# Kernel optimization log

Hardware: AMD Instinct MI355X
Metric: run time of the kernel (lower is better)

The kernel has to match this reference:

```python
import jax, jax.numpy as jnp
import numpy as np

B, A, T, C = 16, 19200, 50, 80
LAMBDA_COORD = 5.0
EPS = 1e-6

def _make_boxes(key, shape):
    k1, k2 = jax.random.split(key)
    xy1 = jax.random.uniform(k1, shape[:-1] + (2,)) * 0.8
    wh = jax.random.uniform(k2, shape[:-1] + (2,)) * 0.2 + 0.01
    return jnp.concatenate([xy1, xy1 + wh], axis=-1)

def setup_inputs() -> dict:
    key = jax.random.key(0)
    ks = jax.random.split(key, 6)
    return {
        'pred_boxes': _make_boxes(ks[0], (B, A, 4)),
        'pred_conf': jax.random.normal(ks[1], (B, A, 1), dtype=jnp.float32),
        'pred_cls': jax.random.normal(ks[2], (B, A, C), dtype=jnp.float32),
        'target_boxes': _make_boxes(ks[3], (B, T, 4)),
        'target_labels': jax.random.randint(ks[4], (B, T), 0, C),
        'anchors': jax.random.uniform(ks[5], (3, 2), dtype=jnp.float32),
    }

def _bce_logits(x, z):
    # BCEWithLogits, reduction='none'
    return jnp.maximum(x, 0.0) - x * z + jnp.log1p(jnp.exp(-jnp.abs(x)))

def _box_iou(b1, b2):
    # b1: [A,4], b2: [T,4] -> [A,T]
    area1 = (b1[:, 2] - b1[:, 0]) * (b1[:, 3] - b1[:, 1])
    area2 = (b2[:, 2] - b2[:, 0]) * (b2[:, 3] - b2[:, 1])
    ix1 = jnp.maximum(b1[:, 0:1], b2[None, :, 0])
    iy1 = jnp.maximum(b1[:, 1:2], b2[None, :, 1])
    ix2 = jnp.minimum(b1[:, 2:3], b2[None, :, 2])
    iy2 = jnp.minimum(b1[:, 3:4], b2[None, :, 3])
    inter = jnp.clip(ix2 - ix1, 0.0) * jnp.clip(iy2 - iy1, 0.0)
    union = area1[:, None] + area2[None, :] - inter
    return inter / (union + EPS)

def _ciou_loss(b1, b2):
    # elementwise CIoU between matched boxes [T,4],[T,4]
    # (original builds pairwise IoU then takes the diagonal == elementwise IoU)
    area1 = (b1[:, 2] - b1[:, 0]) * (b1[:, 3] - b1[:, 1])
    area2 = (b2[:, 2] - b2[:, 0]) * (b2[:, 3] - b2[:, 1])
    iw = jnp.clip(jnp.minimum(b1[:, 2], b2[:, 2]) - jnp.maximum(b1[:, 0], b2[:, 0]), 0.0)
    ih = jnp.clip(jnp.minimum(b1[:, 3], b2[:, 3]) - jnp.maximum(b1[:, 1], b2[:, 1]), 0.0)
    inter = iw * ih
    iou = inter / (area1 + area2 - inter + EPS)
    b1x1, b1y1, b1x2, b1y2 = b1[:, 0], b1[:, 1], b1[:, 2], b1[:, 3]
    b2x1, b2y1, b2x2, b2y2 = b2[:, 0], b2[:, 1], b2[:, 2], b2[:, 3]
    c_diag = (jnp.maximum(b1x2, b2x2) - jnp.minimum(b1x1, b2x1)) ** 2 + \
             (jnp.maximum(b1y2, b2y2) - jnp.minimum(b1y1, b2y1)) ** 2
    center_dist = ((b1x1 + b1x2 - b2x1 - b2x2) / 2) ** 2 + ((b1y1 + b1y2 - b2y1 - b2y2) / 2) ** 2
    w1, h1 = b1x2 - b1x1, b1y2 - b1y1
    w2, h2 = b2x2 - b2x1, b2y2 - b2y1
    v = (4.0 / jnp.pi ** 2) * (jnp.arctan(w2 / h2) - jnp.arctan(w1 / h1)) ** 2
    alpha = v / (1.0 - iou + v + EPS)
    ciou = iou - center_dist / c_diag - alpha * v
    return 1.0 - ciou

def _per_image(pb, pc, pcls, tb, tl):
    # pb:[A,4] pc:[A,1] pcls:[A,C] tb:[T,4] tl:[T]
    ious = _box_iou(pb, tb)                    # [A,T]
    best_idx = jnp.argmax(ious, axis=0)        # [T]
    obj_mask = jnp.zeros((pb.shape[0], 1), pb.dtype).at[best_idx].set(1.0)
    obj_loss = _bce_logits(pc, obj_mask).mean()
    box_loss = _ciou_loss(pb[best_idx], tb).mean()
    tgt_cls = jax.nn.one_hot(tl, pcls.shape[-1], dtype=pcls.dtype)
    cls_loss = _bce_logits(pcls[best_idx], tgt_cls).mean()
    return box_loss, obj_loss, cls_loss

def reference(pred_boxes, pred_conf, pred_cls, target_boxes, target_labels, anchors):
    box_l, obj_l, cls_l = jax.vmap(_per_image)(pred_boxes, pred_conf, pred_cls, target_boxes, target_labels)
    bs = pred_boxes.shape[0]
    total_box = box_l.sum() / bs
    total_obj = obj_l.sum() / bs
    total_cls = cls_l.sum() / bs
    total = LAMBDA_COORD * total_box + total_obj + total_cls
    return total
```

## Files before the change

### kernel.cpp

```cpp
#include <hip/hip_runtime.h>
#include <math.h>

#define NB 16
#define NA 19200
#define NT 50
#define NC 80
#define LAMBDA_COORD 5.0f
#define F_EPS 1e-6f

#define TPG 5
#define NGRP (NT / TPG)
#define KA_BLOCKS (NB * NGRP)
#define KA_THREADS 1024
#define KA_WAVES (KA_THREADS / 64)
#define OBJ_F4_PER_BLK (NB * NA / 4 / KA_BLOCKS)

#define W_OBJ (1.0f / (float)(NB * NA))
#define W_BOX (LAMBDA_COORD / (float)(NB * NT))
#define W_CLS (1.0f / (float)(NB * NT * NC))


__device__ __forceinline__ float bce0(float x) {
    return fmaxf(x, 0.0f) + log1pf(expf(-fabsf(x)));
}

__global__ __launch_bounds__(1024) void kA(
        const float* __restrict__ pb,
        const float* __restrict__ pc,
        const float* __restrict__ pcls,
        const float* __restrict__ tb,
        const int* __restrict__ tl,
        int* __restrict__ best_idx,
        float* __restrict__ part) {
    const float4* pb4 = (const float4*)pb;
    const float4* tb4 = (const float4*)tb;
    const float4* pc4 = (const float4*)pc;

    const int b   = blockIdx.x / NGRP;
    const int g   = blockIdx.x % NGRP;
    const int tid = threadIdx.x;
    const int wave = tid >> 6;
    const int lane = tid & 63;

    float4 t4[TPG];
    float  ta[TPG];
    #pragma unroll
    for (int i = 0; i < TPG; ++i) {
        t4[i] = tb4[b * NT + g * TPG + i];
        ta[i] = (t4[i].z - t4[i].x) * (t4[i].w - t4[i].y) + F_EPS;
    }

    float best[TPG];
    int   bidx[TPG];
    #pragma unroll
    for (int i = 0; i < TPG; ++i) { best[i] = -1.0f; bidx[i] = NA; }

    const size_t boff = (size_t)b * NA;
    int a0 = tid;
    float4 p0 = pb4[boff + a0];
    int a1 = a0 + KA_THREADS;
    bool h1 = a1 < NA;
    float4 p1;
    if (h1) p1 = pb4[boff + a1];

    while (true) {
        const int a2 = a1 + KA_THREADS;
        const bool h2 = h1 && (a2 < NA);
        float4 p2;
        if (h2) p2 = pb4[boff + a2];

        {
            float area1 = (p0.z - p0.x) * (p0.w - p0.y);
            #pragma unroll
            for (int i = 0; i < TPG; ++i) {
                float ix1 = fmaxf(p0.x, t4[i].x), iy1 = fmaxf(p0.y, t4[i].y);
                float ix2 = fminf(p0.z, t4[i].z), iy2 = fminf(p0.w, t4[i].w);
                float inter = fmaxf(ix2 - ix1, 0.0f) * fmaxf(iy2 - iy1, 0.0f);
                float u = area1 + ta[i] - inter;
                float iou = inter * __builtin_amdgcn_rcpf(u);
                if (iou > best[i]) { best[i] = iou; bidx[i] = a0; }
            }
        }

        if (!h1) break;
        p0 = p1; a0 = a1;
        p1 = p2; a1 = a2; h1 = h2;
    }

    __shared__ float swv[KA_WAVES][TPG];
    __shared__ int   swi[KA_WAVES][TPG];
    __shared__ int   sbi5[TPG];
    __shared__ float swred[KA_WAVES];

    #pragma unroll
    for (int i = 0; i < TPG; ++i) {
        float v = best[i];
        int   ix = bidx[i];
        #pragma unroll
        for (int m = 1; m < 64; m <<= 1) {
            float ov = __shfl_xor(v, m);
            int   oi = __shfl_xor(ix, m);
            if (ov > v || (ov == v && oi < ix)) { v = ov; ix = oi; }
        }
        if (lane == 0) { swv[wave][i] = v; swi[wave][i] = ix; }
    }
    __syncthreads();

    if (tid < TPG) {
        float v = swv[0][tid];
        int   ix = swi[0][tid];
        #pragma unroll
        for (int w = 1; w < KA_WAVES; ++w) {
            float ov = swv[w][tid];
            int   oi = swi[w][tid];
            if (ov > v || (ov == v && oi < ix)) { v = ov; ix = oi; }
        }
        best_idx[b * NT + g * TPG + tid] = ix;
        sbi5[tid] = ix;
    }
    __syncthreads();

    float s = 0.0f;

    if (tid < TPG * NC) {
        const int t = tid / NC;
        const int c = tid - t * NC;
        float x = pcls[((size_t)b * NA + sbi5[t]) * NC + c];
        int lab = tl[b * NT + g * TPG + t];
        s += W_CLS * (bce0(x) - (lab == c ? x : 0.0f));
    }

    if (tid >= 512 && tid < 512 + TPG) {
        const int t  = tid - 512;
        const int bi = sbi5[t];
        const float* p  = pb + ((size_t)b * NA + bi) * 4;
        const float* tg = tb + ((size_t)b * NT + g * TPG + t) * 4;
        float b1x1 = p[0],  b1y1 = p[1],  b1x2 = p[2],  b1y2 = p[3];
        float b2x1 = tg[0], b2y1 = tg[1], b2x2 = tg[2], b2y2 = tg[3];

        float area1 = (b1x2 - b1x1) * (b1y2 - b1y1);
        float area2 = (b2x2 - b2x1) * (b2y2 - b2y1);
        float iw = fmaxf(fminf(b1x2, b2x2) - fmaxf(b1x1, b2x1), 0.0f);
        float ih = fmaxf(fminf(b1y2, b2y2) - fmaxf(b1y1, b2y1), 0.0f);
        float inter = iw * ih;
        float iou = inter / (area1 + area2 - inter + F_EPS);

        float cdx = fmaxf(b1x2, b2x2) - fminf(b1x1, b2x1);
        float cdy = fmaxf(b1y2, b2y2) - fminf(b1y1, b2y1);
        float c_diag = cdx * cdx + cdy * cdy;

        float cx = (b1x1 + b1x2 - b2x1 - b2x2) * 0.5f;
        float cy = (b1y1 + b1y2 - b2y1 - b2y2) * 0.5f;
        float center_dist = cx * cx + cy * cy;

        float w1 = b1x2 - b1x1, h1 = b1y2 - b1y1;
        float w2 = b2x2 - b2x1, h2 = b2y2 - b2y1;
        float dat = atanf(w2 / h2) - atanf(w1 / h1);
        float vv = (float)(4.0 / (M_PI * M_PI)) * dat * dat;
        float alpha = vv / (1.0f - iou + vv + F_EPS);
        float ciou = iou - center_dist / c_diag - alpha * vv;
        s += W_BOX * (1.0f - ciou);
    }

    if (tid < OBJ_F4_PER_BLK) {
        float4 v4 = pc4[blockIdx.x * OBJ_F4_PER_BLK + tid];
        s += W_OBJ * (bce0(v4.x) + bce0(v4.y) + bce0(v4.z) + bce0(v4.w));
    }

    #pragma unroll
    for (int m = 32; m > 0; m >>= 1) s += __shfl_down(s, m);
    if (lane == 0) swred[wave] = s;
    __syncthreads();
    if (tid < KA_WAVES) {
        float v = swred[tid];
        #pragma unroll
        for (int m = 8; m > 0; m >>= 1) v += __shfl_down(v, m);
        if (tid == 0) part[blockIdx.x] = v;
    }
}

__global__ __launch_bounds__(256) void kB(
        const float* __restrict__ pc,
        const int* __restrict__ best_idx,
        const float* __restrict__ part,
        float* __restrict__ out) {
    const int tid = threadIdx.x;
    const int wave = tid >> 6;
    const int lane = tid & 63;

    __shared__ int   sbi[NB * NT];
    __shared__ float swred[4];

    for (int i = tid; i < NB * NT; i += 256) sbi[i] = best_idx[i];
    __syncthreads();

    float s = 0.0f;
    if (tid < KA_BLOCKS) s += part[tid];

    for (int i = tid; i < NB * NT; i += 256) {
        const int b = i / NT;
        const int t = i - b * NT;
        const int bi = sbi[i];
        bool dup = false;
        for (int tp = 0; tp < t; ++tp)
            if (sbi[b * NT + tp] == bi) dup = true;
        if (!dup) s -= W_OBJ * pc[(size_t)b * NA + bi];
    }

    #pragma unroll
    for (int m = 32; m > 0; m >>= 1) s += __shfl_down(s, m);
    if (lane == 0) swred[wave] = s;
    __syncthreads();
    if (tid == 0) out[0] = swred[0] + swred[1] + swred[2] + swred[3];
}

extern "C" void kernel_launch(void* const* d_in, const int* in_sizes, int n_in,
                              void* d_out, int out_size, void* d_ws, size_t ws_size,
                              hipStream_t stream) {
    const float* pb   = (const float*)d_in[0];
    const float* pc   = (const float*)d_in[1];
    const float* pcls = (const float*)d_in[2];
    const float* tb   = (const float*)d_in[3];
    const int*   tl   = (const int*)d_in[4];

    char* ws = (char*)d_ws;
    float* part     = (float*)ws;
    int*   best_idx = (int*)(ws + 1024);

    kA<<<KA_BLOCKS, KA_THREADS, 0, stream>>>(pb, pc, pcls, tb, tl, best_idx, part);
    kB<<<1, 256, 0, stream>>>(pc, best_idx, part, (float*)d_out);
}
```

Before: 34.84 us.

## Split anchor scan into halves and move matched-loss work to per-batch second kernel

```diff
diff --git a/kernel.cpp b/kernel.cpp
--- a/kernel.cpp
+++ b/kernel.cpp
@@ -10,7 +10,9 @@
 
 #define TPG 5
 #define NGRP (NT / TPG)
-#define KA_BLOCKS (NB * NGRP)
+#define NHALF 2
+#define HALF_A (NA / NHALF)
+#define KA_BLOCKS (NB * NGRP * NHALF)
 #define KA_THREADS 1024
 #define KA_WAVES (KA_THREADS / 64)
 #define OBJ_F4_PER_BLK (NB * NA / 4 / KA_BLOCKS)
@@ -27,21 +29,26 @@
 __global__ __launch_bounds__(1024) void kA(
         const float* __restrict__ pb,
         const float* __restrict__ pc,
-        const float* __restrict__ pcls,
         const float* __restrict__ tb,
-        const int* __restrict__ tl,
-        int* __restrict__ best_idx,
-        float* __restrict__ part) {
+        float* __restrict__ val_part,
+        int* __restrict__ idx_part,
+        float* __restrict__ part,
+        float* __restrict__ out) {
     const float4* pb4 = (const float4*)pb;
     const float4* tb4 = (const float4*)tb;
     const float4* pc4 = (const float4*)pc;
 
-    const int b   = blockIdx.x / NGRP;
-    const int g   = blockIdx.x % NGRP;
+    const int blk = blockIdx.x;
+    const int b   = blk / (NGRP * NHALF);
+    const int r   = blk % (NGRP * NHALF);
+    const int g   = r / NHALF;
+    const int h   = r % NHALF;
     const int tid = threadIdx.x;
     const int wave = tid >> 6;
     const int lane = tid & 63;
 
+    if (blk == 0 && tid == 0) out[0] = 0.0f;
+
     float4 t4[TPG];
     float  ta[TPG];
     #pragma unroll
@@ -55,22 +62,27 @@
     #pragma unroll
     for (int i = 0; i < TPG; ++i) { best[i] = -1.0f; bidx[i] = NA; }
 
-    const size_t boff = (size_t)b * NA;
+    const size_t boff = (size_t)b * NA + h * HALF_A;
     int a0 = tid;
     float4 p0 = pb4[boff + a0];
     int a1 = a0 + KA_THREADS;
-    bool h1 = a1 < NA;
+    bool v1 = a1 < HALF_A;
     float4 p1;
-    if (h1) p1 = pb4[boff + a1];
+    if (v1) p1 = pb4[boff + a1];
+    int a2 = a1 + KA_THREADS;
+    bool v2 = v1 && (a2 < HALF_A);
+    float4 p2;
+    if (v2) p2 = pb4[boff + a2];
 
     while (true) {
-        const int a2 = a1 + KA_THREADS;
-        const bool h2 = h1 && (a2 < NA);
-        float4 p2;
-        if (h2) p2 = pb4[boff + a2];
+        const int a3 = a2 + KA_THREADS;
+        const bool v3 = v2 && (a3 < HALF_A);
+        float4 p3;
+        if (v3) p3 = pb4[boff + a3];
 
         {
             float area1 = (p0.z - p0.x) * (p0.w - p0.y);
+            const int gidx = h * HALF_A + a0;
             #pragma unroll
             for (int i = 0; i < TPG; ++i) {
                 float ix1 = fmaxf(p0.x, t4[i].x), iy1 = fmaxf(p0.y, t4[i].y);
@@ -78,18 +90,18 @@
                 float inter = fmaxf(ix2 - ix1, 0.0f) * fmaxf(iy2 - iy1, 0.0f);
                 float u = area1 + ta[i] - inter;
                 float iou = inter * __builtin_amdgcn_rcpf(u);
-                if (iou > best[i]) { best[i] = iou; bidx[i] = a0; }
+                if (iou > best[i]) { best[i] = iou; bidx[i] = gidx; }
             }
         }
 
-        if (!h1) break;
+        if (!v1) break;
         p0 = p1; a0 = a1;
-        p1 = p2; a1 = a2; h1 = h2;
+        p1 = p2; a1 = a2; v1 = v2;
+        p2 = p3; a2 = a3; v2 = v3;
     }
 
     __shared__ float swv[KA_WAVES][TPG];
     __shared__ int   swi[KA_WAVES][TPG];
-    __shared__ int   sbi5[TPG];
     __shared__ float swred[KA_WAVES];
 
     #pragma unroll
@@ -115,26 +127,77 @@
             int   oi = swi[w][tid];
             if (ov > v || (ov == v && oi < ix)) { v = ov; ix = oi; }
         }
-        best_idx[b * NT + g * TPG + tid] = ix;
-        sbi5[tid] = ix;
-    }
-    __syncthreads();
+        const int t = b * NT + g * TPG + tid;
+        val_part[t * 2 + h] = v;
+        idx_part[t * 2 + h] = ix;
+    }
 
     float s = 0.0f;
-
-    if (tid < TPG * NC) {
-        const int t = tid / NC;
-        const int c = tid - t * NC;
-        float x = pcls[((size_t)b * NA + sbi5[t]) * NC + c];
-        int lab = tl[b * NT + g * TPG + t];
-        s += W_CLS * (bce0(x) - (lab == c ? x : 0.0f));
-    }
-
-    if (tid >= 512 && tid < 512 + TPG) {
-        const int t  = tid - 512;
-        const int bi = sbi5[t];
+    if (tid < OBJ_F4_PER_BLK) {
+        float4 v4 = pc4[blk * OBJ_F4_PER_BLK + tid];
+        s = W_OBJ * (bce0(v4.x) + bce0(v4.y) + bce0(v4.z) + bce0(v4.w));
+    }
+    #pragma unroll
+    for (int m = 32; m > 0; m >>= 1) s += __shfl_down(s, m);
+    if (lane == 0) swred[wave] = s;
+    __syncthreads();
+    if (tid < KA_WAVES) {
+        float v = swred[tid];
+        #pragma unroll
+        for (int m = 8; m > 0; m >>= 1) v += __shfl_down(v, m);
+        if (tid == 0) part[blk] = v;
+    }
+}
+
+__global__ __launch_bounds__(256) void kB(
+        const float* __restrict__ pb,
+        const float* __restrict__ pc,
+        const float* __restrict__ pcls,
+        const float* __restrict__ tb,
+        const int* __restrict__ tl,
+        const float* __restrict__ val_part,
+        const int* __restrict__ idx_part,
+        const float* __restrict__ part,
+        float* __restrict__ out) {
+    const int b   = blockIdx.x;
+    const int tid = threadIdx.x;
+    const int wave = tid >> 6;
+    const int lane = tid & 63;
+
+    __shared__ int   sbi[NT];
+    __shared__ int   slab[NT];
+    __shared__ float swred[4];
+
+    if (tid < NT) {
+        const int t = b * NT + tid;
+        float v0 = val_part[t * 2 + 0]; int i0 = idx_part[t * 2 + 0];
+        float v1 = val_part[t * 2 + 1]; int i1 = idx_part[t * 2 + 1];
+        sbi[tid]  = (v1 > v0 || (v1 == v0 && i1 < i0)) ? i1 : i0;
+        slab[tid] = tl[b * NT + tid];
+    }
+    __syncthreads();
+
+    float s = 0.0f;
+
+    if (tid < NGRP * NHALF) s += part[b * NGRP * NHALF + tid];
+
+    for (int i = tid; i < NT * NC; i += 256) {
+        const int t = i / NC;
+        const int c = i - t * NC;
+        float x = pcls[((size_t)b * NA + sbi[t]) * NC + c];
+        s += W_CLS * (bce0(x) - (slab[t] == c ? x : 0.0f));
+    }
+
+    if (tid < NT) {
+        const int bi = sbi[tid];
+
+        bool dup = false;
+        for (int tp = 0; tp < tid; ++tp)
+            if (sbi[tp] == bi) dup = true;
+        if (!dup) s -= W_OBJ * pc[(size_t)b * NA + bi];
+
         const float* p  = pb + ((size_t)b * NA + bi) * 4;
-        const float* tg = tb + ((size_t)b * NT + g * TPG + t) * 4;
+        const float* tg = tb + ((size_t)b * NT + tid) * 4;
         float b1x1 = p[0],  b1y1 = p[1],  b1x2 = p[2],  b1y2 = p[3];
         float b2x1 = tg[0], b2y1 = tg[1], b2x2 = tg[2], b2y2 = tg[3];
 
@@ -162,56 +225,11 @@
         s += W_BOX * (1.0f - ciou);
     }
 
-    if (tid < OBJ_F4_PER_BLK) {
-        float4 v4 = pc4[blockIdx.x * OBJ_F4_PER_BLK + tid];
-        s += W_OBJ * (bce0(v4.x) + bce0(v4.y) + bce0(v4.z) + bce0(v4.w));
-    }
-
     #pragma unroll
     for (int m = 32; m > 0; m >>= 1) s += __shfl_down(s, m);
     if (lane == 0) swred[wave] = s;
     __syncthreads();
-    if (tid < KA_WAVES) {
-        float v = swred[tid];
-        #pragma unroll
-        for (int m = 8; m > 0; m >>= 1) v += __shfl_down(v, m);
-        if (tid == 0) part[blockIdx.x] = v;
-    }
-}
-
-__global__ __launch_bounds__(256) void kB(
-        const float* __restrict__ pc,
-        const int* __restrict__ best_idx,
-        const float* __restrict__ part,
-        float* __restrict__ out) {
-    const int tid = threadIdx.x;
-    const int wave = tid >> 6;
-    const int lane = tid & 63;
-
-    __shared__ int   sbi[NB * NT];
-    __shared__ float swred[4];
-
-    for (int i = tid; i < NB * NT; i += 256) sbi[i] = best_idx[i];
-    __syncthreads();
-
-    float s = 0.0f;
-    if (tid < KA_BLOCKS) s += part[tid];
-
-    for (int i = tid; i < NB * NT; i += 256) {
-        const int b = i / NT;
-        const int t = i - b * NT;
-        const int bi = sbi[i];
-        bool dup = false;
-        for (int tp = 0; tp < t; ++tp)
-            if (sbi[b * NT + tp] == bi) dup = true;
-        if (!dup) s -= W_OBJ * pc[(size_t)b * NA + bi];
-    }
-
-    #pragma unroll
-    for (int m = 32; m > 0; m >>= 1) s += __shfl_down(s, m);
-    if (lane == 0) swred[wave] = s;
-    __syncthreads();
-    if (tid == 0) out[0] = swred[0] + swred[1] + swred[2] + swred[3];
+    if (tid == 0) atomicAdd(out, swred[0] + swred[1] + swred[2] + swred[3]);
 }
 
 extern "C" void kernel_launch(void* const* d_in, const int* in_sizes, int n_in,
@@ -225,8 +243,11 @@
 
     char* ws = (char*)d_ws;
     float* part     = (float*)ws;
-    int*   best_idx = (int*)(ws + 1024);
-
-    kA<<<KA_BLOCKS, KA_THREADS, 0, stream>>>(pb, pc, pcls, tb, tl, best_idx, part);
-    kB<<<1, 256, 0, stream>>>(pc, best_idx, part, (float*)d_out);
-}
+    float* val_part = (float*)(ws + 2048);
+    int*   idx_part = (int*)(ws + 8448);
+
+    kA<<<KA_BLOCKS, KA_THREADS, 0, stream>>>(
+        pb, pc, tb, val_part, idx_part, part, (float*)d_out);
+    kB<<<NB, 256, 0, stream>>>(
+        pb, pc, pcls, tb, tl, val_part, idx_part, part, (float*)d_out);
+}
```

New measurement: 36.36 us. 1.04x slower.
